# Kernel tuning notes

Measured on AMD Instinct MI355X. Metric: run time of the kernel, lower is better.

The kernel has to match this reference:

```python
import jax, jax.numpy as jnp
import numpy as np

W_PULL = 1.0
W_PUSH = 1.0
W_NORM = 0.001
W_EDGE = 10.0
DELTA_V = 0.5
DELTA_D = 1.5
CE_W = 1.0
DICE_W = 1.0
IGN = -100
NUM_CLASSES = 8
EMBED_DIM = 16
NUM_INST = 16  # instance ids 1..16, 0 = background
EPS_C = 1e-8
EPS_D = 1e-5


def setup_inputs() -> dict:
    key = jax.random.key(0)
    k1, k2, k3, k4 = jax.random.split(key, 4)
    B, D, H, W = 2, 64, 128, 128
    return {
        "sem_logits": jax.random.normal(k1, (B, NUM_CLASSES, D, H, W), jnp.float32),
        "instance_embed": jax.random.normal(k2, (B, EMBED_DIM, D, H, W), jnp.float32),
        "class_labels": jax.random.randint(k3, (B, D, H, W), 0, NUM_CLASSES, dtype=jnp.int32),
        "labels": jax.random.randint(k4, (B, D, H, W), 0, NUM_INST + 1, dtype=jnp.int32),
    }


def _ce_loss(logits, target):
    # nn.CrossEntropyLoss(ignore_index=-100), mean over valid voxels
    logp = jax.nn.log_softmax(logits, axis=1)
    valid = (target != IGN)
    t_safe = jnp.where(valid, target, 0)
    nll = -jnp.take_along_axis(logp, t_safe[:, None].astype(jnp.int32), axis=1)[:, 0]
    v = valid.astype(logits.dtype)
    return (nll * v).sum() / jnp.maximum(v.sum(), 1.0)


def _dice_loss(logits, target):
    C = logits.shape[1]
    probs = jax.nn.softmax(logits, axis=1)
    valid = (target != IGN)
    t_safe = jnp.where(valid, target, 0)
    one_hot = jax.nn.one_hot(t_safe, C, dtype=probs.dtype, axis=1)  # [B,C,D,H,W]
    vm = valid[:, None].astype(probs.dtype)
    probs = probs * vm
    one_hot = one_hot * vm
    axes = tuple(range(2, probs.ndim))
    inter = (probs * one_hot).sum(axes)
    card_p = probs.sum(axes)
    card_g = one_hot.sum(axes)
    dice = (2.0 * inter + EPS_D) / (card_p + card_g + EPS_D)
    return 1.0 - dice.mean()


def _boundary_weight(labels):
    # morphological gradient: 3x3x3 max-pool minus min-pool, replicate pad
    lf = labels.astype(jnp.float32)
    p = jnp.pad(lf, ((0, 0), (1, 1), (1, 1), (1, 1)), mode='edge')
    mx = jax.lax.reduce_window(p, -jnp.inf, jax.lax.max, (1, 3, 3, 3), (1, 1, 1, 1), 'VALID')
    mn = jax.lax.reduce_window(p, jnp.inf, jax.lax.min, (1, 3, 3, 3), (1, 1, 1, 1), 'VALID')
    boundary = (mx != mn).astype(jnp.float32)
    return 1.0 + boundary * (W_EDGE - 1.0)


def _instance_loss(embed, labels, w):
    B, C = embed.shape[:2]
    e_flat = embed.reshape(B, C, -1)   # [B,C,N]
    l_flat = labels.reshape(B, -1)     # [B,N]
    w_flat = w.reshape(B, -1)          # [B,N] (w_bone == 1 since weight_bone==1.0)
    K = NUM_INST

    def per_batch(e, l, wv):
        seg = lambda x: jax.ops.segment_sum(x, l, num_segments=K + 1)
        wsum = seg(wv)                       # [K+1]
        cnt = seg(jnp.ones_like(wv))         # [K+1]
        cnum = seg((e * wv).T)               # [K+1, C]
        centers = cnum / (wsum[:, None] + EPS_C)
        cg = centers[l]                      # [N, C] gather own-instance center
        dist = jnp.linalg.norm(e.T - cg, axis=-1)
        pull_sum = seg(jax.nn.relu(dist - DELTA_V) ** 2 * wv)
        present = cnt[1:] > 0                # ids 1..K
        loss_pull = jnp.where(present, pull_sum[1:] / jnp.maximum(cnt[1:], 1.0), 0.0).sum()
        c = centers[1:]                      # [K, C]
        iu, ju = jnp.triu_indices(K, k=1)
        pw = jnp.linalg.norm(c[iu] - c[ju], axis=-1)
        pv = (present[iu] & present[ju]).astype(pw.dtype)
        npres = present.sum().astype(pw.dtype)
        npairs = npres * (npres - 1.0) / 2.0
        push = jax.nn.relu(2.0 * DELTA_D - pw) ** 2 * pv
        loss_push = jnp.where(npairs > 0, push.sum() / jnp.maximum(npairs, 1.0), 0.0)
        cn = jnp.linalg.norm(c, axis=-1)
        loss_norm = jnp.where(npres > 0, (cn * present).sum() / jnp.maximum(npres, 1.0), 0.0)
        return loss_pull, loss_push, loss_norm, (npres > 0).astype(jnp.float32)

    lp, lpu, ln, val = jax.vmap(per_batch)(e_flat, l_flat, w_flat)
    n = jnp.maximum(val.sum(), 1.0)
    return (W_PULL * lp.sum() + W_PUSH * lpu.sum() + W_NORM * ln.sum()) / n


def reference(sem_logits, instance_embed, class_labels, labels):
    loss_ce = _ce_loss(sem_logits, class_labels)
    loss_dice = _dice_loss(sem_logits, class_labels)
    loss_sem = CE_W * loss_ce + DICE_W * loss_dice
    w_edge = _boundary_weight(labels)
    # weight_bone == 1.0 -> w_bone = ones (scipy EDT branch disabled by module guard)
    loss_ins = _instance_loss(instance_embed, labels, w_edge)
    loss = loss_sem + loss_ins
    return loss, loss_sem, loss_ce, loss_dice, loss_ins
```

## Files before the change

### kernel.cpp

```cpp
#include <hip/hip_runtime.h>

#define DHW (64*128*128)
#define MIR 32

#define OFF_CEM   0
#define OFF_SEGM  1568
#define OFF_PULLM 21152
#define OFF_CTR   22240
#define OFF_CNT   22784
#define ACC_FLOATS 22818

typedef __bf16 bf16x8 __attribute__((ext_vector_type(8)));
typedef float f32x4 __attribute__((ext_vector_type(4)));
union FragU { short s[8]; bf16x8 v; };

__device__ inline short f2bf(float f) {
    union { float f; unsigned u; } v; v.f = f;
    unsigned r = v.u + 0x7FFF + ((v.u >> 16) & 1);
    return (short)(r >> 16);
}

__device__ inline unsigned edge4(const int* __restrict__ L, int vb, int4 c) {
    int x = vb & 127, y = (vb >> 7) & 127, z = vb >> 14;
    int z0 = max(z - 1, 0), z1 = min(z + 1, 63);
    int y0 = max(y - 1, 0), y1 = min(y + 1, 127);
    int xm = max(x - 1, 0), xp = min(x + 4, 127);
    unsigned b0 = 0, b1 = 0, b2 = 0, b3 = 0;
    for (int zz = z0; zz <= z1; ++zz) {
        for (int yy = y0; yy <= y1; ++yy) {
            const int* row = L + (zz << 14) + (yy << 7);
            int4 r = *reinterpret_cast<const int4*>(&row[x]);
            int rm = row[xm], rp = row[xp];
            b0 |= (rm != c.x) | (r.x != c.x) | (r.y != c.x);
            b1 |= (r.x != c.y) | (r.y != c.y) | (r.z != c.y);
            b2 |= (r.y != c.z) | (r.z != c.z) | (r.w != c.z);
            b3 |= (r.z != c.w) | (r.w != c.w) | (rp != c.w);
            if (b0 & b1 & b2 & b3) return 0xF;
        }
    }
    return b0 | (b1 << 1) | (b2 << 2) | (b3 << 3);
}

__global__ void zero_kernel(float* acc) {
    int i = blockIdx.x * 1024 + threadIdx.x;
    if (i < ACC_FLOATS) acc[i] = 0.0f;
}

__device__ void ce_role(const float* __restrict__ logits, const int* __restrict__ cls,
                        float* __restrict__ acc, int b, int blk, float* sh) {
    int tid = threadIdx.x;
    int mir = blk & (MIR - 1);
    int vb = (blk * 256 + tid) * 4;
    const float* lg = logits + (size_t)b * 8 * DHW;
    const int* cl = cls + (size_t)b * DHW;

    float4 xc[8];
#pragma unroll
    for (int c = 0; c < 8; ++c)
        xc[c] = *reinterpret_cast<const float4*>(&lg[(size_t)c * DHW + vb]);
    int4 t4 = *reinterpret_cast<const int4*>(&cl[vb]);
    int tt[4] = {t4.x, t4.y, t4.z, t4.w};

    float nll = 0.f, cardp[8], inter[8], cardg[8];
#pragma unroll
    for (int c = 0; c < 8; ++c) { cardp[c] = 0.f; inter[c] = 0.f; cardg[c] = 0.f; }

#pragma unroll
    for (int j = 0; j < 4; ++j) {
        float x[8];
#pragma unroll
        for (int c = 0; c < 8; ++c) x[c] = ((const float*)&xc[c])[j];
        int t = tt[j];
        bool valid = (t != -100);
        float mx = x[0];
#pragma unroll
        for (int c = 1; c < 8; ++c) mx = fmaxf(mx, x[c]);
        float e[8], s = 0.f;
#pragma unroll
        for (int c = 0; c < 8; ++c) { e[c] = __expf(x[c] - mx); s += e[c]; }
        float inv = 1.0f / s;
        float lse = __logf(s);
        if (valid) {
#pragma unroll
            for (int c = 0; c < 8; ++c) {
                float p = e[c] * inv;
                cardp[c] += p;
                if (t == c) { inter[c] += p; cardg[c] += 1.f; nll += mx + lse - x[c]; }
            }
        }
    }

    if (tid < 25) sh[tid] = 0.f;
    __syncthreads();
    int lane = tid & 63;
    float vals[25];
    vals[0] = nll;
#pragma unroll
    for (int c = 0; c < 8; ++c) { vals[1 + c] = cardp[c]; vals[9 + c] = inter[c]; vals[17 + c] = cardg[c]; }
#pragma unroll
    for (int i = 0; i < 25; ++i) {
        float r = vals[i];
#pragma unroll
        for (int off = 32; off > 0; off >>= 1) r += __shfl_down(r, off, 64);
        if (lane == 0) atomicAdd(&sh[i], r);
    }
    __syncthreads();
    if (tid < 25) {
        int dst;
        if (tid == 0) dst = 0;
        else if (tid < 9) dst = 1 + b * 8 + (tid - 1);
        else if (tid < 17) dst = 17 + b * 8 + (tid - 9);
        else dst = 33 + b * 8 + (tid - 17);
        atomicAdd(&acc[OFF_CEM + mir * 49 + dst], sh[tid]);
    }
}

__global__ __launch_bounds__(256) void phaseA_kernel(const float* __restrict__ logits,
                                                     const float* __restrict__ embed,
                                                     const int* __restrict__ cls,
                                                     const int* __restrict__ labels,
                                                     float* __restrict__ acc) {
    __shared__ float smem[352];
    int x = blockIdx.x;
    int g = x / 3, r3 = x % 3;
    int tid = threadIdx.x;

    if (r3 == 2) {
        int ce_idx = g;
        ce_role(logits, cls, acc, ce_idx >> 9, (ce_idx & 511), smem);
        return;
    }
    int seg_idx = g * 2 + r3;
    int b = seg_idx & 1;
    int blk = seg_idx >> 1;
    int mir = blk & (MIR - 1);
    int lane = tid & 63;
    int wv = tid >> 6;
    int m = lane & 15;
    int quad = lane >> 4;

    const int* L = labels + (size_t)b * DHW;
    const float* E = embed + (size_t)b * 16 * DHW + (size_t)m * DHW;

    int waveId = blk * 4 + wv;
    int wavebase = waveId * 256;

    unsigned eb_own;
    {
        int own_off = wavebase + lane * 4;
        int4 lo = *reinterpret_cast<const int4*>(&L[own_off]);
        eb_own = edge4(L, own_off, lo);
    }

    int off = wavebase + quad * 8;

    f32x4 acc_c = {0.f, 0.f, 0.f, 0.f};
    f32x4 acc_w = {0.f, 0.f, 0.f, 0.f};
    f32x4 acc_n = {0.f, 0.f, 0.f, 0.f};

    FragU ones_col;
#pragma unroll
    for (int j = 0; j < 8; ++j) ones_col.s[j] = (m == 0) ? (short)0x3F80 : (short)0;

    int4 l0 = *reinterpret_cast<const int4*>(&L[off]);
    int4 l1 = *reinterpret_cast<const int4*>(&L[off + 4]);
    float4 f0 = *reinterpret_cast<const float4*>(&E[off]);
    float4 f1 = *reinterpret_cast<const float4*>(&E[off + 4]);

    for (int i = 0; i < 8; ++i) {
        int4 nl0, nl1; float4 nf0, nf1;
        if (i < 7) {
            int noff = off + 32;
            nl0 = *reinterpret_cast<const int4*>(&L[noff]);
            nl1 = *reinterpret_cast<const int4*>(&L[noff + 4]);
            nf0 = *reinterpret_cast<const float4*>(&E[noff]);
            nf1 = *reinterpret_cast<const float4*>(&E[noff + 4]);
        }
        int s0 = i * 8 + quad * 2;
        unsigned ebA = (unsigned)__shfl((int)eb_own, s0, 64);
        unsigned ebB = (unsigned)__shfl((int)eb_own, s0 + 1, 64);
        unsigned eb = (ebA & 0xF) | ((ebB & 0xF) << 4);

        int ls[8] = {l0.x, l0.y, l0.z, l0.w, l1.x, l1.y, l1.z, l1.w};
        float fs[8] = {f0.x, f0.y, f0.z, f0.w, f1.x, f1.y, f1.z, f1.w};

        FragU a, a2, bf;
#pragma unroll
        for (int j = 0; j < 8; ++j) {
            short w = ((eb >> j) & 1) ? (short)0x4120 : (short)0x3F80;
            bool hit = (ls[j] == m + 1);
            a.s[j]  = hit ? w : (short)0;
            a2.s[j] = hit ? (short)0x3F80 : (short)0;
            bf.s[j] = f2bf(fs[j]);
        }
        acc_c = __builtin_amdgcn_mfma_f32_16x16x32_bf16(a.v, bf.v, acc_c, 0, 0, 0);
        acc_w = __builtin_amdgcn_mfma_f32_16x16x32_bf16(a.v, ones_col.v, acc_w, 0, 0, 0);
        acc_n = __builtin_amdgcn_mfma_f32_16x16x32_bf16(a2.v, ones_col.v, acc_n, 0, 0, 0);

        l0 = nl0; l1 = nl1; f0 = nf0; f1 = nf1;
        off += 32;
    }

    float* cacc = smem;
    for (int i = tid; i < 288; i += 256) cacc[i] = 0.f;
    __syncthreads();
#pragma unroll
    for (int r = 0; r < 4; ++r)
        atomicAdd(&cacc[(quad * 4 + r) * 16 + m], acc_c[r]);
    if (m == 0) {
#pragma unroll
        for (int r = 0; r < 4; ++r) {
            atomicAdd(&cacc[256 + quad * 4 + r], acc_w[r]);
            atomicAdd(&cacc[272 + quad * 4 + r], acc_n[r]);
        }
    }
    __syncthreads();
    {
        float* segbase = acc + OFF_SEGM + mir * 612 + b * 306;
        atomicAdd(&segbase[16 + tid], cacc[tid]);
        if (tid < 16) atomicAdd(&segbase[272 + 1 + tid], cacc[256 + tid]);
        else if (tid < 32) atomicAdd(&segbase[289 + 1 + (tid - 16)], cacc[256 + tid]);
    }
}

__global__ __launch_bounds__(1024) void centers_kernel(float* acc) {
    int tid = threadIdx.x;
    if (tid < 544) {
        int b = tid / 272, r = tid % 272;
        int k = r >> 4;
        float cn = 0.f, ws = 0.f;
        for (int mv = 0; mv < MIR; ++mv) {
            const float* segbase = acc + OFF_SEGM + mv * 612 + b * 306;
            if (r >= 16) cn += segbase[r];
            ws += segbase[272 + k];
        }
        acc[OFF_CTR + tid] = (r >= 16) ? cn / (ws + 1e-8f) : 0.f;
    } else if (tid < 578) {
        int j = tid - 544;
        int b = j / 17, k = j % 17;
        float s = 0.f;
        for (int mv = 0; mv < MIR; ++mv)
            s += acc[OFF_SEGM + mv * 612 + b * 306 + 289 + k];
        acc[OFF_CNT + j] = s;
    }
}

__global__ __launch_bounds__(256) void phaseB_kernel(const float* __restrict__ logits,
                                                     const float* __restrict__ embed,
                                                     const int* __restrict__ cls,
                                                     const int* __restrict__ labels,
                                                     float* __restrict__ acc) {
    __shared__ float smem[352];
    int x = blockIdx.x;
    int g = x / 3, r3 = x % 3;
    int tid = threadIdx.x;

    if (r3 == 2) {
        int ce_idx = g;
        ce_role(logits, cls, acc, ce_idx >> 9, (ce_idx & 511) + 512, smem);
        return;
    }
    int pull_idx = g * 2 + r3;
    int b = pull_idx & 1;
    int blk = pull_idx >> 1;
    int wv = tid >> 6;
    float* ctr = smem;
    float* ps = smem + 272;
    for (int i = tid; i < 272; i += 256) ctr[i] = acc[OFF_CTR + b * 272 + i];
    for (int i = tid; i < 80; i += 256) ps[i] = 0.f;
    __syncthreads();

    const int* L = labels + (size_t)b * DHW;
    const float* E = embed + (size_t)b * 16 * DHW;
    int vb = (blk * 256 + tid) * 4;

    int4 l4 = *reinterpret_cast<const int4*>(&L[vb]);
    int l[4] = {l4.x, l4.y, l4.z, l4.w};
    unsigned eb = edge4(L, vb, l4);

    float d2a[4] = {0.f, 0.f, 0.f, 0.f};
#pragma unroll
    for (int q = 0; q < 4; ++q) {
        float4 e0 = *reinterpret_cast<const float4*>(&E[(size_t)(4 * q + 0) * DHW + vb]);
        float4 e1 = *reinterpret_cast<const float4*>(&E[(size_t)(4 * q + 1) * DHW + vb]);
        float4 e2 = *reinterpret_cast<const float4*>(&E[(size_t)(4 * q + 2) * DHW + vb]);
        float4 e3 = *reinterpret_cast<const float4*>(&E[(size_t)(4 * q + 3) * DHW + vb]);
#pragma unroll
        for (int j = 0; j < 4; ++j) {
            if (l[j] != 0) {
                float4 cv = *reinterpret_cast<const float4*>(&ctr[l[j] * 16 + q * 4]);
                float d0 = ((const float*)&e0)[j] - cv.x;
                float d1 = ((const float*)&e1)[j] - cv.y;
                float d2 = ((const float*)&e2)[j] - cv.z;
                float d3 = ((const float*)&e3)[j] - cv.w;
                d2a[j] += d0 * d0 + d1 * d1 + d2 * d2 + d3 * d3;
            }
        }
    }

#pragma unroll
    for (int j = 0; j < 4; ++j) {
        if (l[j] != 0) {
            float w = ((eb >> j) & 1) ? 10.f : 1.f;
            float d = fmaxf(sqrtf(d2a[j]) - 0.5f, 0.f);
            atomicAdd(&ps[wv * 20 + l[j]], d * d * w);
        }
    }
    __syncthreads();
    if (tid >= 1 && tid < 17) {
        float v = ps[tid] + ps[20 + tid] + ps[40 + tid] + ps[60 + tid];
        int mir = blk & (MIR - 1);
        if (v != 0.f) atomicAdd(&acc[OFF_PULLM + mir * 34 + b * 17 + tid], v);
    }
}

__global__ __launch_bounds__(256) void finalize_kernel(const float* __restrict__ acc, float* __restrict__ out) {
    __shared__ float s_ce[49], s_pl[34];
    __shared__ float sh_push[2], sh_norm[2], sh_pull[2], sh_npres[2];
    int tid = threadIdx.x;
    if (tid < 49) {
        float s = 0.f;
        for (int mv = 0; mv < MIR; ++mv) s += acc[OFF_CEM + mv * 49 + tid];
        s_ce[tid] = s;
    }
    if (tid >= 64 && tid < 98) {
        int j = tid - 64;
        float s = 0.f;
        for (int mv = 0; mv < MIR; ++mv) s += acc[OFF_PULLM + mv * 34 + j];
        s_pl[j] = s;
    }
    if (tid < 2) { sh_push[tid] = 0.f; sh_norm[tid] = 0.f; sh_pull[tid] = 0.f; sh_npres[tid] = 0.f; }
    __syncthreads();

    if (tid < 32) {
        int b = tid >> 4, k = (tid & 15) + 1;
        float cnt = acc[OFF_CNT + b * 17 + k];
        if (cnt > 0.f) {
            atomicAdd(&sh_npres[b], 1.f);
            atomicAdd(&sh_pull[b], s_pl[b * 17 + k] / fmaxf(cnt, 1.f));
            const float* c = &acc[OFF_CTR + (b * 17 + k) * 16];
            float n2 = 0.f;
            for (int i = 0; i < 16; ++i) n2 += c[i] * c[i];
            atomicAdd(&sh_norm[b], sqrtf(n2));
        }
    }
    for (int t = tid; t < 240; t += blockDim.x) {
        int b = t / 120, p = t % 120;
        int i = 1, rem = p;
        while (rem >= (16 - i)) { rem -= (16 - i); ++i; }
        int j = i + 1 + rem;
        bool pi = acc[OFF_CNT + b * 17 + i] > 0.f;
        bool pj = acc[OFF_CNT + b * 17 + j] > 0.f;
        if (pi && pj) {
            const float* ci = &acc[OFF_CTR + (b * 17 + i) * 16];
            const float* cj = &acc[OFF_CTR + (b * 17 + j) * 16];
            float d2 = 0.f;
            for (int c = 0; c < 16; ++c) { float dd = ci[c] - cj[c]; d2 += dd * dd; }
            float r = fmaxf(3.0f - sqrtf(d2), 0.f);
            atomicAdd(&sh_push[b], r * r);
        }
    }
    __syncthreads();
    if (tid == 0) {
        float nll = s_ce[0];
        float vcnt = 0.f;
        for (int i = 0; i < 16; ++i) vcnt += s_ce[33 + i];
        float ce = nll / fmaxf(vcnt, 1.f);
        float dsum = 0.f;
        for (int i = 0; i < 16; ++i) {
            float it = s_ce[17 + i], cp = s_ce[1 + i], cg = s_ce[33 + i];
            dsum += (2.f * it + 1e-5f) / (cp + cg + 1e-5f);
        }
        float dice = 1.f - dsum / 16.f;
        float lp = 0.f, lpu = 0.f, ln = 0.f, val = 0.f;
        for (int b = 0; b < 2; ++b) {
            float npres = sh_npres[b];
            lp += sh_pull[b];
            float npairs = npres * (npres - 1.f) * 0.5f;
            lpu += (npairs > 0.f) ? sh_push[b] / fmaxf(npairs, 1.f) : 0.f;
            ln += (npres > 0.f) ? sh_norm[b] / fmaxf(npres, 1.f) : 0.f;
            val += (npres > 0.f) ? 1.f : 0.f;
        }
        float n = fmaxf(val, 1.f);
        float ins = (1.0f * lp + 1.0f * lpu + 0.001f * ln) / n;
        float sem = ce + dice;
        out[0] = sem + ins;
        out[1] = sem;
        out[2] = ce;
        out[3] = dice;
        out[4] = ins;
    }
}

extern "C" void kernel_launch(void* const* d_in, const int* in_sizes, int n_in,
                              void* d_out, int out_size, void* d_ws, size_t ws_size,
                              hipStream_t stream) {
    const float* sem = (const float*)d_in[0];
    const float* emb = (const float*)d_in[1];
    const int* cls = (const int*)d_in[2];
    const int* lab = (const int*)d_in[3];
    float* out = (float*)d_out;
    float* acc = (float*)d_ws;

    hipLaunchKernelGGL(zero_kernel, dim3(23), dim3(1024), 0, stream, acc);
    hipLaunchKernelGGL(phaseA_kernel, dim3(3072), dim3(256), 0, stream, sem, emb, cls, lab, acc);
    hipLaunchKernelGGL(centers_kernel, dim3(1), dim3(1024), 0, stream, acc);
    hipLaunchKernelGGL(phaseB_kernel, dim3(3072), dim3(256), 0, stream, sem, emb, cls, lab, acc);
    hipLaunchKernelGGL(finalize_kernel, dim3(1), dim3(256), 0, stream, acc, out);
}
```

Baseline: 305.0 us.

## Cache edge bits from phase A and rebalance CE work across phases

Phase A now writes each voxel group's 4-bit boundary mask to workspace bytes, and phase B reads that byte instead of recomputing the 27-neighbour stencil. The CE blocks are redistributed unevenly between the two phases (fewer in A, more in B) so the lighter phase B takes more CE work. The edge4 loops are fully unrolled with clamped indices and lose the early exit, and the phase A load loop gets double-buffered prefetch two steps ahead. The cost is an extra byte store and load per voxel group plus reliance on workspace space beyond the accumulators.

```diff
diff --git a/kernel.cpp b/kernel.cpp
--- a/kernel.cpp
+++ b/kernel.cpp
@@ -9,6 +9,7 @@
 #define OFF_CTR   22240
 #define OFF_CNT   22784
 #define ACC_FLOATS 22818
+#define OFF_EDGE_BYTES 92160
 
 typedef __bf16 bf16x8 __attribute__((ext_vector_type(8)));
 typedef float f32x4 __attribute__((ext_vector_type(4)));
@@ -22,12 +23,14 @@
 
 __device__ inline unsigned edge4(const int* __restrict__ L, int vb, int4 c) {
     int x = vb & 127, y = (vb >> 7) & 127, z = vb >> 14;
-    int z0 = max(z - 1, 0), z1 = min(z + 1, 63);
-    int y0 = max(y - 1, 0), y1 = min(y + 1, 127);
     int xm = max(x - 1, 0), xp = min(x + 4, 127);
     unsigned b0 = 0, b1 = 0, b2 = 0, b3 = 0;
-    for (int zz = z0; zz <= z1; ++zz) {
-        for (int yy = y0; yy <= y1; ++yy) {
+#pragma unroll
+    for (int dz = -1; dz <= 1; ++dz) {
+        int zz = min(max(z + dz, 0), 63);
+#pragma unroll
+        for (int dy = -1; dy <= 1; ++dy) {
+            int yy = min(max(y + dy, 0), 127);
             const int* row = L + (zz << 14) + (yy << 7);
             int4 r = *reinterpret_cast<const int4*>(&row[x]);
             int rm = row[xm], rp = row[xp];
@@ -35,7 +38,6 @@
             b1 |= (r.x != c.y) | (r.y != c.y) | (r.z != c.y);
             b2 |= (r.y != c.z) | (r.z != c.z) | (r.w != c.z);
             b3 |= (r.z != c.w) | (r.w != c.w) | (rp != c.w);
-            if (b0 & b1 & b2 & b3) return 0xF;
         }
     }
     return b0 | (b1 << 1) | (b2 << 2) | (b3 << 3);
@@ -122,15 +124,17 @@
                                                      float* __restrict__ acc) {
     __shared__ float smem[352];
     int x = blockIdx.x;
-    int g = x / 3, r3 = x % 3;
+    int g = x / 11, r = x % 11;
     int tid = threadIdx.x;
 
-    if (r3 == 2) {
-        int ce_idx = g;
-        ce_role(logits, cls, acc, ce_idx >> 9, (ce_idx & 511), smem);
+    if (r >= 8) {
+        int ce_idx = g * 3 + (r - 8);
+        int b = (ce_idx >= 384) ? 1 : 0;
+        int blk = ce_idx - b * 384;
+        ce_role(logits, cls, acc, b, blk, smem);
         return;
     }
-    int seg_idx = g * 2 + r3;
+    int seg_idx = g * 8 + r;
     int b = seg_idx & 1;
     int blk = seg_idx >> 1;
     int mir = blk & (MIR - 1);
@@ -151,6 +155,10 @@
         int4 lo = *reinterpret_cast<const int4*>(&L[own_off]);
         eb_own = edge4(L, own_off, lo);
     }
+    {
+        unsigned char* EB = (unsigned char*)acc + OFF_EDGE_BYTES + ((size_t)b << 18);
+        EB[blk * 256 + tid] = (unsigned char)eb_own;
+    }
 
     int off = wavebase + quad * 8;
 
@@ -162,27 +170,41 @@
 #pragma unroll
     for (int j = 0; j < 8; ++j) ones_col.s[j] = (m == 0) ? (short)0x3F80 : (short)0;
 
-    int4 l0 = *reinterpret_cast<const int4*>(&L[off]);
-    int4 l1 = *reinterpret_cast<const int4*>(&L[off + 4]);
-    float4 f0 = *reinterpret_cast<const float4*>(&E[off]);
-    float4 f1 = *reinterpret_cast<const float4*>(&E[off + 4]);
-
+    int4 La0 = *reinterpret_cast<const int4*>(&L[off]);
+    int4 La1 = *reinterpret_cast<const int4*>(&L[off + 4]);
+    float4 Fa0 = *reinterpret_cast<const float4*>(&E[off]);
+    float4 Fa1 = *reinterpret_cast<const float4*>(&E[off + 4]);
+    int4 Lb0 = *reinterpret_cast<const int4*>(&L[off + 32]);
+    int4 Lb1 = *reinterpret_cast<const int4*>(&L[off + 36]);
+    float4 Fb0 = *reinterpret_cast<const float4*>(&E[off + 32]);
+    float4 Fb1 = *reinterpret_cast<const float4*>(&E[off + 36]);
+
+#pragma unroll
     for (int i = 0; i < 8; ++i) {
-        int4 nl0, nl1; float4 nf0, nf1;
-        if (i < 7) {
-            int noff = off + 32;
-            nl0 = *reinterpret_cast<const int4*>(&L[noff]);
-            nl1 = *reinterpret_cast<const int4*>(&L[noff + 4]);
-            nf0 = *reinterpret_cast<const float4*>(&E[noff]);
-            nf1 = *reinterpret_cast<const float4*>(&E[noff + 4]);
+        int4 cl0, cl1; float4 cf0, cf1;
+        if (i & 1) { cl0 = Lb0; cl1 = Lb1; cf0 = Fb0; cf1 = Fb1; }
+        else       { cl0 = La0; cl1 = La1; cf0 = Fa0; cf1 = Fa1; }
+        if (i < 6) {
+            int noff = off + (i + 2) * 32;
+            if (i & 1) {
+                Lb0 = *reinterpret_cast<const int4*>(&L[noff]);
+                Lb1 = *reinterpret_cast<const int4*>(&L[noff + 4]);
+                Fb0 = *reinterpret_cast<const float4*>(&E[noff]);
+                Fb1 = *reinterpret_cast<const float4*>(&E[noff + 4]);
+            } else {
+                La0 = *reinterpret_cast<const int4*>(&L[noff]);
+                La1 = *reinterpret_cast<const int4*>(&L[noff + 4]);
+                Fa0 = *reinterpret_cast<const float4*>(&E[noff]);
+                Fa1 = *reinterpret_cast<const float4*>(&E[noff + 4]);
+            }
         }
         int s0 = i * 8 + quad * 2;
         unsigned ebA = (unsigned)__shfl((int)eb_own, s0, 64);
         unsigned ebB = (unsigned)__shfl((int)eb_own, s0 + 1, 64);
         unsigned eb = (ebA & 0xF) | ((ebB & 0xF) << 4);
 
-        int ls[8] = {l0.x, l0.y, l0.z, l0.w, l1.x, l1.y, l1.z, l1.w};
-        float fs[8] = {f0.x, f0.y, f0.z, f0.w, f1.x, f1.y, f1.z, f1.w};
+        int ls[8] = {cl0.x, cl0.y, cl0.z, cl0.w, cl1.x, cl1.y, cl1.z, cl1.w};
+        float fs[8] = {cf0.x, cf0.y, cf0.z, cf0.w, cf1.x, cf1.y, cf1.z, cf1.w};
 
         FragU a, a2, bf;
 #pragma unroll
@@ -196,22 +218,19 @@
         acc_c = __builtin_amdgcn_mfma_f32_16x16x32_bf16(a.v, bf.v, acc_c, 0, 0, 0);
         acc_w = __builtin_amdgcn_mfma_f32_16x16x32_bf16(a.v, ones_col.v, acc_w, 0, 0, 0);
         acc_n = __builtin_amdgcn_mfma_f32_16x16x32_bf16(a2.v, ones_col.v, acc_n, 0, 0, 0);
-
-        l0 = nl0; l1 = nl1; f0 = nf0; f1 = nf1;
-        off += 32;
     }
 
     float* cacc = smem;
     for (int i = tid; i < 288; i += 256) cacc[i] = 0.f;
     __syncthreads();
 #pragma unroll
-    for (int r = 0; r < 4; ++r)
-        atomicAdd(&cacc[(quad * 4 + r) * 16 + m], acc_c[r]);
+    for (int rr = 0; rr < 4; ++rr)
+        atomicAdd(&cacc[(quad * 4 + rr) * 16 + m], acc_c[rr]);
     if (m == 0) {
 #pragma unroll
-        for (int r = 0; r < 4; ++r) {
-            atomicAdd(&cacc[256 + quad * 4 + r], acc_w[r]);
-            atomicAdd(&cacc[272 + quad * 4 + r], acc_n[r]);
+        for (int rr = 0; rr < 4; ++rr) {
+            atomicAdd(&cacc[256 + quad * 4 + rr], acc_w[rr]);
+            atomicAdd(&cacc[272 + quad * 4 + rr], acc_n[rr]);
         }
     }
     __syncthreads();
@@ -252,15 +271,17 @@
                                                      float* __restrict__ acc) {
     __shared__ float smem[352];
     int x = blockIdx.x;
-    int g = x / 3, r3 = x % 3;
+    int g = x / 13, r = x % 13;
     int tid = threadIdx.x;
 
-    if (r3 == 2) {
-        int ce_idx = g;
-        ce_role(logits, cls, acc, ce_idx >> 9, (ce_idx & 511) + 512, smem);
+    if (r >= 8) {
+        int ce_idx = g * 5 + (r - 8);
+        int b = (ce_idx >= 640) ? 1 : 0;
+        int blk = 384 + (ce_idx - b * 640);
+        ce_role(logits, cls, acc, b, blk, smem);
         return;
     }
-    int pull_idx = g * 2 + r3;
+    int pull_idx = g * 8 + r;
     int b = pull_idx & 1;
     int blk = pull_idx >> 1;
     int wv = tid >> 6;
@@ -276,7 +297,11 @@
 
     int4 l4 = *reinterpret_cast<const int4*>(&L[vb]);
     int l[4] = {l4.x, l4.y, l4.z, l4.w};
-    unsigned eb = edge4(L, vb, l4);
+    unsigned eb;
+    {
+        const unsigned char* EB = (const unsigned char*)acc + OFF_EDGE_BYTES + ((size_t)b << 18);
+        eb = EB[blk * 256 + tid];
+    }
 
     float d2a[4] = {0.f, 0.f, 0.f, 0.f};
 #pragma unroll
@@ -403,8 +428,8 @@
     float* acc = (float*)d_ws;
 
     hipLaunchKernelGGL(zero_kernel, dim3(23), dim3(1024), 0, stream, acc);
-    hipLaunchKernelGGL(phaseA_kernel, dim3(3072), dim3(256), 0, stream, sem, emb, cls, lab, acc);
+    hipLaunchKernelGGL(phaseA_kernel, dim3(2816), dim3(256), 0, stream, sem, emb, cls, lab, acc);
     hipLaunchKernelGGL(centers_kernel, dim3(1), dim3(1024), 0, stream, acc);
-    hipLaunchKernelGGL(phaseB_kernel, dim3(3072), dim3(256), 0, stream, sem, emb, cls, lab, acc);
+    hipLaunchKernelGGL(phaseB_kernel, dim3(3328), dim3(256), 0, stream, sem, emb, cls, lab, acc);
     hipLaunchKernelGGL(finalize_kernel, dim3(1), dim3(256), 0, stream, acc, out);
 }
```

Result: no change. 307.5 us (+0.8%).
